# Optimization experiments

Measured on AMD Instinct MI355X. Metric: run time of the kernel, lower is better.

## Reference

```python
import jax, jax.numpy as jnp
import numpy as np

H = 512      # hidden_size
V = 50257    # vocab_size
B = 64       # batch
T = 512      # sequence length


def setup_inputs() -> dict:
    key = jax.random.key(0)
    k1, k2, k3, k4 = jax.random.split(key, 4)
    # Parameters as constructed in HMM.__init__ (row-stochastic / log-normalized)
    alpha_exp = jax.nn.softmax(jax.random.normal(k1, (H, H), dtype=jnp.float32), axis=-1)
    beta = jax.nn.log_softmax(jax.random.normal(k2, (H, V), dtype=jnp.float32), axis=-1)
    gamma_exp = jax.nn.softmax(jax.random.normal(k3, (1, H), dtype=jnp.float32), axis=-1)
    input_ids = jax.random.randint(k4, (B, T), 0, V)
    return {"alpha_exp": alpha_exp, "beta": beta, "gamma_exp": gamma_exp, "input_ids": input_ids}


def _stable_mvm(log_W, log_x):
    # log-space matvec: log(W @ x) with max-shift stabilization (matches torch stable_mvm)
    x_max = jnp.max(log_x)
    x = jnp.exp(log_x - x_max)                       # (H,)
    w_max = jnp.max(log_W, axis=1, keepdims=True)    # (H,1)
    W = jnp.exp(log_W - w_max)                       # (H,H)
    z = W @ x                                        # (H,)
    return jnp.log(z) + x_max + jnp.squeeze(w_max, -1)


def reference(alpha_exp, beta, gamma_exp, input_ids):
    # HMM.compute_forward_probability
    logA_T = jnp.log(alpha_exp + 1e-12).T            # (H,H) transposed transition log-probs
    alpha0 = jnp.log(gamma_exp) + beta[:, input_ids[:, 0]].T   # (B,H)
    mvm = jax.vmap(_stable_mvm, in_axes=(None, 0))

    def step(alpha_prev, x_t):
        a = mvm(logA_T, alpha_prev) + beta[:, x_t].T  # (B,H)
        return a, None

    alpha_final, _ = jax.lax.scan(step, alpha0, input_ids[:, 1:].T)
    return alpha_final
```

## Files before the change

kernel.cpp:

```cpp
#include <hip/hip_runtime.h>
#include <hip/hip_bf16.h>

#define HH 512
#define VV 50257
#define TL 512
#define NT 512
#define DYN_LDS 98304

typedef __attribute__((ext_vector_type(4))) float floatx4;
typedef __attribute__((ext_vector_type(8))) int intx8;

__device__ __forceinline__ unsigned short f2bf(float f) {
  union { float f; unsigned int u; } v; v.f = f;
  unsigned int r = (v.u + 0x7fffu + ((v.u >> 16) & 1u)) >> 16;
  return (unsigned short)r;
}
__device__ __forceinline__ float bf2f(unsigned short h) {
  union { unsigned int u; float f; } v; v.u = ((unsigned int)h) << 16;
  return v.f;
}

__device__ __forceinline__ float wave_max_dpp(float x) {
  int xi = __builtin_bit_cast(int, x);
#define DPPSTEP(ctrl)                                                              \
  {                                                                                \
    int yi = __builtin_amdgcn_update_dpp(xi, xi, (ctrl), 0xf, 0xf, false);         \
    float a = __builtin_bit_cast(float, xi), b = __builtin_bit_cast(float, yi);    \
    xi = __builtin_bit_cast(int, fmaxf(a, b));                                     \
  }
  DPPSTEP(0xB1)
  DPPSTEP(0x4E)
  DPPSTEP(0x141)
  DPPSTEP(0x140)
  DPPSTEP(0x142)
  DPPSTEP(0x143)
#undef DPPSTEP
  return __builtin_bit_cast(float, __builtin_amdgcn_readlane(xi, 63));
}

__global__ void colmaxK(const float* __restrict__ A, float* __restrict__ cmax) {
  __shared__ float red[4][64];
  int x = threadIdx.x & 63;
  int y = threadIdx.x >> 6;
  int c = blockIdx.x * 64 + x;
  float m = -INFINITY;
  for (int j = y; j < HH; j += 4) m = fmaxf(m, A[j * HH + c]);
  red[y][x] = m;
  __syncthreads();
  if (y == 0)
    cmax[c] = fmaxf(fmaxf(red[0][x], red[1][x]), fmaxf(red[2][x], red[3][x])) + 1e-12f;
}

__global__ void buildWf8sK(const float* __restrict__ A, const float* __restrict__ cmax,
                           intx8* __restrict__ Wf8s) {
  int gid = blockIdx.x * 256 + threadIdx.x;
  int L = gid & 63, r = gid >> 6;
  int kk = r & 3, T = r >> 2;
  int n = T * 16 + (L & 15);
  int kbase = kk * 128 + (L >> 4) * 32;
  float inv = 1.0f / cmax[n];
  intx8 o;
#pragma unroll
  for (int d = 0; d < 8; ++d) {
    float v0 = (A[(kbase + 4 * d + 0) * HH + n] + 1e-12f) * inv;
    float v1 = (A[(kbase + 4 * d + 1) * HH + n] + 1e-12f) * inv;
    float v2 = (A[(kbase + 4 * d + 2) * HH + n] + 1e-12f) * inv;
    float v3 = (A[(kbase + 4 * d + 3) * HH + n] + 1e-12f) * inv;
    unsigned pk;
    asm("v_cvt_pk_fp8_f32 %0, %1, %2" : "=v"(pk) : "v"(v0), "v"(v1));
    asm("v_cvt_pk_fp8_f32 %0, %1, %2 op_sel:[0,0,1]" : "+v"(pk) : "v"(v2), "v"(v3));
    o[d] = (int)pk;
  }
  Wf8s[gid] = o;
}

__global__ void buildPtab(const float* __restrict__ beta, const float* __restrict__ cmax,
                          unsigned short* __restrict__ Ptab) {
  __shared__ float tile[32][33];
  int v0 = blockIdx.x * 32, h0 = blockIdx.y * 32;
  int tx = threadIdx.x, ty = threadIdx.y;
#pragma unroll
  for (int k = 0; k < 4; ++k) {
    int v = v0 + tx;
    if (v < VV) tile[ty + 8 * k][tx] = beta[(h0 + ty + 8 * k) * VV + v];
  }
  __syncthreads();
  float cm = cmax[h0 + tx];
#pragma unroll
  for (int k = 0; k < 4; ++k) {
    int v = v0 + ty + 8 * k;
    if (v < VV) Ptab[(long)v * HH + h0 + tx] = f2bf(__expf(tile[tx][ty + 8 * k]) * cm);
  }
}

__global__ __launch_bounds__(NT, 2) __attribute__((amdgpu_waves_per_eu(2, 2)))
void hmm_main(const intx8* __restrict__ Wf8s,
              const unsigned short* __restrict__ Ptab,
              const float* __restrict__ gamma,
              const float* __restrict__ cmax,
              const int* __restrict__ ids,
              float* __restrict__ out) {
  extern __shared__ char dls[];
  unsigned char* xbuf = (unsigned char*)dls;
  float* wmx = (float*)(dls + 1024);
  int* ids_l = (int*)(dls + 1088);

  const int b = blockIdx.x, tid = threadIdx.x;
  const int w = tid >> 6, L = tid & 63;
  const int q = L >> 4;
  const long bT = (long)b * TL;

  ids_l[tid] = ids[bT + tid];

  intx8 wa[4][4];
#pragma unroll
  for (int tau = 0; tau < 4; ++tau)
#pragma unroll
    for (int kk = 0; kk < 4; ++kk)
      wa[tau][kk] = Wf8s[((4 * w + tau) * 4 + kk) * 64 + L];

  const int n = tid;
  float A;

  {
    const int id0 = ids[bT];
    float u0 = gamma[n] * bf2f(Ptab[(long)id0 * HH + n]) / cmax[n];
    float m = wave_max_dpp(u0);
    if (L == 0) wmx[w] = m;
    __syncthreads();
    float4 ga = *(const float4*)wmx, gb = *(const float4*)(wmx + 4);
    float M = fmaxf(fmaxf(fmaxf(ga.x, ga.y), fmaxf(ga.z, ga.w)),
                    fmaxf(fmaxf(gb.x, gb.y), fmaxf(gb.z, gb.w)));
    M = fmaxf(M, 1e-30f);
    A = __logf(M);
    float x0 = u0 * __builtin_amdgcn_rcpf(M);
    unsigned pk;
    asm("v_cvt_pk_fp8_f32 %0, %1, %2" : "=v"(pk) : "v"(x0), "v"(x0));
    xbuf[n] = (unsigned char)(pk & 0xff);
    __syncthreads();
  }

  unsigned short pvc = Ptab[(long)ids_l[1] * HH + n];

  for (int t = 1; t < TL; ++t) {
    const int idn = ids_l[(t + 1 < TL) ? (t + 1) : t];
    const unsigned short pvn = Ptab[(long)idn * HH + n];

    const unsigned char* xb = xbuf + ((t - 1) & 1) * 512;

    floatx4 acc[4];
#pragma unroll
    for (int tau = 0; tau < 4; ++tau) acc[tau] = (floatx4){0.f, 0.f, 0.f, 0.f};

    __builtin_amdgcn_s_setprio(1);
#pragma unroll
    for (int kk = 0; kk < 4; ++kk) {
      intx8 af = *(const intx8*)(xb + kk * 128 + q * 32);
#pragma unroll
      for (int tau = 0; tau < 4; ++tau)
        acc[tau] = __builtin_amdgcn_mfma_scale_f32_16x16x128_f8f6f4(
            af, wa[tau][kk], acc[tau], 0, 0, 0, 0x7F7F7F7F, 0, 0x7F7F7F7F);
    }
    __builtin_amdgcn_s_setprio(0);

    const float z = (q < 2) ? (q == 0 ? acc[0][0] : acc[1][0])
                            : (q == 2 ? acc[2][0] : acc[3][0]);
    const float un = z * bf2f(pvc);

    if (t == TL - 1) {
      out[(long)b * HH + n] = __logf(fmaxf(un, 1e-37f)) + A;
    } else {
      float m = wave_max_dpp(un);
      if (L == 0) wmx[w] = m;
      asm volatile("s_waitcnt lgkmcnt(0)" ::: "memory");
      __builtin_amdgcn_s_barrier();
      __builtin_amdgcn_sched_barrier(0);
      float4 ga = *(const float4*)wmx, gb = *(const float4*)(wmx + 4);
      float G = fmaxf(fmaxf(fmaxf(ga.x, ga.y), fmaxf(ga.z, ga.w)),
                      fmaxf(fmaxf(gb.x, gb.y), fmaxf(gb.z, gb.w)));
      G = fmaxf(G, 1e-30f);
      A += __logf(G);
      float x = un * __builtin_amdgcn_rcpf(G);
      unsigned pk;
      asm("v_cvt_pk_fp8_f32 %0, %1, %2" : "=v"(pk) : "v"(x), "v"(x));
      xbuf[(t & 1) * 512 + n] = (unsigned char)(pk & 0xff);
      asm volatile("s_waitcnt lgkmcnt(0)" ::: "memory");
      __builtin_amdgcn_s_barrier();
      __builtin_amdgcn_sched_barrier(0);
    }
    pvc = pvn;
  }
}

extern "C" void kernel_launch(void* const* d_in, const int* in_sizes, int n_in,
                              void* d_out, int out_size, void* d_ws, size_t ws_size,
                              hipStream_t stream) {
  const float* alpha_exp = (const float*)d_in[0];
  const float* beta = (const float*)d_in[1];
  const float* gamma = (const float*)d_in[2];
  const int* ids = (const int*)d_in[3];
  float* out = (float*)d_out;

  char* ws = (char*)d_ws;
  float* cmax = (float*)(ws + 0);
  intx8* Wf8s = (intx8*)(ws + 4096);
  unsigned short* Ptab = (unsigned short*)(ws + 528384);

  (void)hipFuncSetAttribute((const void*)hmm_main,
                            hipFuncAttributeMaxDynamicSharedMemorySize, DYN_LDS);

  colmaxK<<<8, 256, 0, stream>>>(alpha_exp, cmax);
  buildWf8sK<<<32, 256, 0, stream>>>(alpha_exp, cmax, Wf8s);
  dim3 gT((VV + 31) / 32, HH / 32), bTd(32, 8);
  buildPtab<<<gT, bTd, 0, stream>>>(beta, cmax, Ptab);

  hmm_main<<<64, NT, DYN_LDS, stream>>>(Wf8s, Ptab, gamma, cmax, ids, out);
}
```

Before: 673.9 us.

## Replace block-wide max barrier with per-wave exponent scaling via MFMA scale operands

Each wave now normalizes its slice of the state vector by a power-of-two taken from its own wave max, instead of waiting on a block-wide max. Per-wave exponents go to LDS next to the fp8 vector, and the next step folds them into the MX scale operands of the scaled MFMA. The running log offset is accumulated from the block max exponent. This removes one of the two barriers per time step, at the cost of extra integer work and possible precision loss for waves whose exponent sits far below the maximum.

```diff
diff --git a/kernel.cpp b/kernel.cpp
--- a/kernel.cpp
+++ b/kernel.cpp
@@ -102,7 +102,7 @@
               float* __restrict__ out) {
   extern __shared__ char dls[];
   unsigned char* xbuf = (unsigned char*)dls;
-  float* wmx = (float*)(dls + 1024);
+  int* elds = (int*)(dls + 1024);
   int* ids_l = (int*)(dls + 1088);
 
   const int b = blockIdx.x, tid = threadIdx.x;
@@ -120,23 +120,19 @@
       wa[tau][kk] = Wf8s[((4 * w + tau) * 4 + kk) * 64 + L];
 
   const int n = tid;
-  float A;
+  float A = 0.f;
 
   {
     const int id0 = ids[bT];
     float u0 = gamma[n] * bf2f(Ptab[(long)id0 * HH + n]) / cmax[n];
     float m = wave_max_dpp(u0);
-    if (L == 0) wmx[w] = m;
-    __syncthreads();
-    float4 ga = *(const float4*)wmx, gb = *(const float4*)(wmx + 4);
-    float M = fmaxf(fmaxf(fmaxf(ga.x, ga.y), fmaxf(ga.z, ga.w)),
-                    fmaxf(fmaxf(gb.x, gb.y), fmaxf(gb.z, gb.w)));
-    M = fmaxf(M, 1e-30f);
-    A = __logf(M);
-    float x0 = u0 * __builtin_amdgcn_rcpf(M);
+    int ebits = (__builtin_bit_cast(int, m) >> 23) & 0xFF;
+    float nf = __builtin_bit_cast(float, (254 - ebits) << 23);
+    float x0 = u0 * nf;
     unsigned pk;
     asm("v_cvt_pk_fp8_f32 %0, %1, %2" : "=v"(pk) : "v"(x0), "v"(x0));
     xbuf[n] = (unsigned char)(pk & 0xff);
+    if (L == 0) elds[w] = ebits - 127;
     __syncthreads();
   }
 
@@ -146,7 +142,27 @@
     const int idn = ids_l[(t + 1 < TL) ? (t + 1) : t];
     const unsigned short pvn = Ptab[(long)idn * HH + n];
 
-    const unsigned char* xb = xbuf + ((t - 1) & 1) * 512;
+    const int pr = (t - 1) & 1;
+    const unsigned char* xb = xbuf + pr * 512;
+
+    int4 ea = *(const int4*)&elds[pr * 8];
+    int4 eb = *(const int4*)&elds[pr * 8 + 4];
+    int E = max(max(max(ea.x, ea.y), max(ea.z, ea.w)),
+                max(max(eb.x, eb.y), max(eb.z, eb.w)));
+    A += (float)E * 0.69314718056f;
+    const int s0 = max(127 + ea.x - E, 0), s1 = max(127 + ea.y - E, 0);
+    const int s2 = max(127 + ea.z - E, 0), s3 = max(127 + ea.w - E, 0);
+    const int s4 = max(127 + eb.x - E, 0), s5 = max(127 + eb.y - E, 0);
+    const int s6 = max(127 + eb.z - E, 0), s7 = max(127 + eb.w - E, 0);
+    const int sa0 = s0 * 0x0101 + s1 * 0x01010000;
+    const int sa1 = s2 * 0x0101 + s3 * 0x01010000;
+    const int sa2 = s4 * 0x0101 + s5 * 0x01010000;
+    const int sa3 = s6 * 0x0101 + s7 * 0x01010000;
+
+    intx8 af0 = *(const intx8*)(xb + 0 * 128 + q * 32);
+    intx8 af1 = *(const intx8*)(xb + 1 * 128 + q * 32);
+    intx8 af2 = *(const intx8*)(xb + 2 * 128 + q * 32);
+    intx8 af3 = *(const intx8*)(xb + 3 * 128 + q * 32);
 
     floatx4 acc[4];
 #pragma unroll
@@ -154,12 +170,15 @@
 
     __builtin_amdgcn_s_setprio(1);
 #pragma unroll
-    for (int kk = 0; kk < 4; ++kk) {
-      intx8 af = *(const intx8*)(xb + kk * 128 + q * 32);
-#pragma unroll
-      for (int tau = 0; tau < 4; ++tau)
-        acc[tau] = __builtin_amdgcn_mfma_scale_f32_16x16x128_f8f6f4(
-            af, wa[tau][kk], acc[tau], 0, 0, 0, 0x7F7F7F7F, 0, 0x7F7F7F7F);
+    for (int tau = 0; tau < 4; ++tau) {
+      acc[tau] = __builtin_amdgcn_mfma_scale_f32_16x16x128_f8f6f4(
+          af0, wa[tau][0], acc[tau], 0, 0, 0, sa0, 0, 0x7F7F7F7F);
+      acc[tau] = __builtin_amdgcn_mfma_scale_f32_16x16x128_f8f6f4(
+          af1, wa[tau][1], acc[tau], 0, 0, 0, sa1, 0, 0x7F7F7F7F);
+      acc[tau] = __builtin_amdgcn_mfma_scale_f32_16x16x128_f8f6f4(
+          af2, wa[tau][2], acc[tau], 0, 0, 0, sa2, 0, 0x7F7F7F7F);
+      acc[tau] = __builtin_amdgcn_mfma_scale_f32_16x16x128_f8f6f4(
+          af3, wa[tau][3], acc[tau], 0, 0, 0, sa3, 0, 0x7F7F7F7F);
     }
     __builtin_amdgcn_s_setprio(0);
 
@@ -171,19 +190,13 @@
       out[(long)b * HH + n] = __logf(fmaxf(un, 1e-37f)) + A;
     } else {
       float m = wave_max_dpp(un);
-      if (L == 0) wmx[w] = m;
-      asm volatile("s_waitcnt lgkmcnt(0)" ::: "memory");
-      __builtin_amdgcn_s_barrier();
-      __builtin_amdgcn_sched_barrier(0);
-      float4 ga = *(const float4*)wmx, gb = *(const float4*)(wmx + 4);
-      float G = fmaxf(fmaxf(fmaxf(ga.x, ga.y), fmaxf(ga.z, ga.w)),
-                      fmaxf(fmaxf(gb.x, gb.y), fmaxf(gb.z, gb.w)));
-      G = fmaxf(G, 1e-30f);
-      A += __logf(G);
-      float x = un * __builtin_amdgcn_rcpf(G);
+      int ebits = (__builtin_bit_cast(int, m) >> 23) & 0xFF;
+      float nf = __builtin_bit_cast(float, (254 - ebits) << 23);
+      float x = un * nf;
       unsigned pk;
       asm("v_cvt_pk_fp8_f32 %0, %1, %2" : "=v"(pk) : "v"(x), "v"(x));
       xbuf[(t & 1) * 512 + n] = (unsigned char)(pk & 0xff);
+      if (L == 0) elds[(t & 1) * 8 + w] = ebits - 127;
       asm volatile("s_waitcnt lgkmcnt(0)" ::: "memory");
       __builtin_amdgcn_s_barrier();
       __builtin_amdgcn_sched_barrier(0);
```

New measurement: 623.9 us. 7.4% less time.
